# Kernel optimization log

Measured on AMD Instinct MI355X. Metric: run time of the kernel, lower is better.

Reference implementation:

```python
import jax, jax.numpy as jnp
import numpy as np

NUM_HEADS = 12

def _rotate_half(t):
    t1, t2 = jnp.split(t, 2, axis=-1)
    return jnp.concatenate([-t2, t1], axis=-1)

def _rope_apply(t, sin, cos):
    # t: [B,H,N,Dh]; sin/cos: [N,Dh] broadcast over B,H
    return t * cos + _rotate_half(t) * sin


def setup_inputs() -> dict:
    key = jax.random.key(0)
    ks = jax.random.split(key, 6)
    B, N, D = 2, 2048, 768
    Dh = D // NUM_HEADS
    return {
        "x": jax.random.normal(ks[0], (B, N, D), dtype=jnp.float32),
        "sin": jax.random.uniform(ks[1], (N, Dh), dtype=jnp.float32),
        "cos": jax.random.uniform(ks[2], (N, Dh), dtype=jnp.float32),
        "qkv_w": jax.random.normal(ks[3], (3 * D, D), dtype=jnp.float32) * (D ** -0.5),
        "proj_w": jax.random.normal(ks[4], (D, D), dtype=jnp.float32) * (D ** -0.5),
        "proj_b": jax.random.normal(ks[5], (D,), dtype=jnp.float32),
    }


def reference(x, sin, cos, qkv_w, proj_w, proj_b):
    B, N, D = x.shape
    H = NUM_HEADS
    Dh = D // H
    scale = Dh ** -0.5
    # fused QKV projection (qkv_bias=False)
    qkv = jnp.einsum("bnd,ed->bne", x, qkv_w)              # [B,N,3D]
    qkv = qkv.reshape(B, N, 3, H, Dh)
    q = jnp.transpose(qkv[:, :, 0], (0, 2, 1, 3))          # [B,H,N,Dh]
    k = jnp.transpose(qkv[:, :, 1], (0, 2, 1, 3))
    v = jnp.transpose(qkv[:, :, 2], (0, 2, 1, 3))
    # inline RoPE (prefix = 0: sin/cos cover all N positions)
    q = _rope_apply(q, sin, cos)
    k = _rope_apply(k, sin, cos)
    # scaled dot-product attention
    scores = jnp.einsum("bhqd,bhkd->bhqk", q, k) * scale   # [B,H,N,N]
    attn = jax.nn.softmax(scores, axis=-1)
    out = jnp.einsum("bhqk,bhkd->bhqd", attn, v)           # [B,H,N,Dh]
    out = jnp.transpose(out, (0, 2, 1, 3)).reshape(B, N, D)
    # output projection
    return jnp.einsum("bnd,ed->bne", out, proj_w) + proj_b
```

## Files before the change

kernel.cpp:

```cpp
#include <hip/hip_runtime.h>
#include <hip/hip_bf16.h>
#include <stdint.h>


typedef unsigned short u16;
typedef __attribute__((ext_vector_type(8))) short s16x8;
typedef __attribute__((ext_vector_type(4))) float f32x4;

#define MFMA16(a, b, c) __builtin_amdgcn_mfma_f32_16x16x32_bf16((a), (b), (c), 0, 0, 0)

__device__ __forceinline__ u16 f2bf(float f) {
    uint32_t u = __float_as_uint(f);
    u = u + 0x7fffu + ((u >> 16) & 1u);
    return (u16)(u >> 16);
}
__device__ __forceinline__ uint32_t pk2(float lo, float hi) {
    return (uint32_t)f2bf(lo) | ((uint32_t)f2bf(hi) << 16);
}
__device__ __forceinline__ float fexp2(float x) { return __builtin_amdgcn_exp2f(x); }

__device__ __forceinline__ void gload16(const void* g, void* l) {
    __builtin_amdgcn_global_load_lds(
        (const __attribute__((address_space(1))) unsigned int*)g,
        (__attribute__((address_space(3))) unsigned int*)l,
        16, 0, 0);
}

__global__ __launch_bounds__(256)
void k_cvt(const float* __restrict__ src, u16* __restrict__ dst, int n4)
{
    const int i = blockIdx.x * 256 + threadIdx.x;
    if (i < n4) {
        const float4 v = ((const float4*)src)[i];
        ushort4 o;
        o.x = f2bf(v.x); o.y = f2bf(v.y); o.z = f2bf(v.z); o.w = f2bf(v.w);
        ((ushort4*)dst)[i] = o;
    }
}

__global__ __launch_bounds__(256, 2)
void k_qkv_rope(const u16* __restrict__ X,
                const u16* __restrict__ W,
                const float* __restrict__ SIN,
                const float* __restrict__ COS,
                u16* __restrict__ qws, u16* __restrict__ kws, u16* __restrict__ vtws)
{
    __shared__ u16 smem[17408];
    u16* const As0 = smem;
    u16* const Bs0 = smem + 8192;

    const int t  = threadIdx.x;
    const int l  = t & 63;
    const int w  = t >> 6;
    const int cl = l & 15, gh = l >> 4;
    const int brow = blockIdx.x * 128;
    const int bcol = blockIdx.y * 128;
    const int wr = (w >> 1) * 64;
    const int wc = (w & 1) * 64;

    const int srow = w * 16 + (l >> 2);
    const int scol = (((l & 3) ^ ((l >> 3) & 3)) * 8);
    const u16* gA = X + (size_t)(brow + srow) * 768 + scol;
    const u16* gB = W + (size_t)(bcol + srow) * 768 + scol;

    const int csw = ((cl >> 1) & 3);

    f32x4 acc[4][4] = {};

    gload16(gA,            As0 + w * 512);
    gload16(gA + 64 * 768, As0 + 2048 + w * 512);
    gload16(gB,            Bs0 + w * 512);
    gload16(gB + 64 * 768, Bs0 + 2048 + w * 512);
    __syncthreads();

    for (int kt = 0; kt < 24; ++kt) {
        const int cur = kt & 1;
        if (kt + 1 < 24) {
            const int k0 = (kt + 1) * 32;
            u16* An = As0 + (cur ^ 1) * 4096;
            u16* Bn = Bs0 + (cur ^ 1) * 4096;
            gload16(gA + k0,            An + w * 512);
            gload16(gA + k0 + 64 * 768, An + 2048 + w * 512);
            gload16(gB + k0,            Bn + w * 512);
            gload16(gB + k0 + 64 * 768, Bn + 2048 + w * 512);
        }
        const char* Ac = (const char*)(As0 + cur * 4096);
        const char* Bc = (const char*)(Bs0 + cur * 4096);
        s16x8 af[4], bv[4];
        #pragma unroll
        for (int m = 0; m < 4; ++m) {
            const int row = wr + m * 16 + cl;
            af[m] = *(const s16x8*)(Ac + row * 64 + ((gh ^ csw) << 4));
        }
        #pragma unroll
        for (int n = 0; n < 4; ++n) {
            const int row = wc + n * 16 + cl;
            bv[n] = *(const s16x8*)(Bc + row * 64 + ((gh ^ csw) << 4));
        }
        #pragma unroll
        for (int m = 0; m < 4; ++m)
            #pragma unroll
            for (int n = 0; n < 4; ++n)
                acc[m][n] = MFMA16(af[m], bv[n], acc[m][n]);
        __syncthreads();
    }

    if (blockIdx.y >= 12) {
        u16* const Vt = smem;
        #pragma unroll
        for (int m = 0; m < 4; ++m)
            #pragma unroll
            for (int jj = 0; jj < 4; ++jj) {
                const int rowl = wr + m * 16 + gh * 4 + jj;
                #pragma unroll
                for (int n = 0; n < 4; ++n)
                    Vt[(wc + n * 16 + cl) * 136 + rowl] = f2bf(acc[m][n][jj]);
            }
        __syncthreads();
        const int dhcol = t >> 1;
        const int c     = t & 1;
        const int gcol  = bcol + dhcol;
        const int h     = (gcol >> 6) - 24;
        const int dh    = gcol & 63;
        const int b     = brow >> 11;
        const int tok0  = (brow & 2047) + c * 64;
        u16* dst = vtws + ((size_t)(b * 12 + h) * 64 + dh) * 2048 + tok0;
        const uint4* src = (const uint4*)((const char*)Vt + dhcol * 272 + c * 128);
        #pragma unroll
        for (int j = 0; j < 8; ++j)
            ((uint4*)dst)[j] = src[j];
    } else {
        const int seg   = (bcol + wc) >> 6;
        const int which = seg / 12;
        const int h     = seg % 12;
        const float qscl = (which == 0) ? 0.1803368801111244f : 1.0f;
        u16* outp = (which == 0) ? qws : kws;

        #pragma unroll
        for (int m = 0; m < 4; ++m) {
            #pragma unroll
            for (int jj = 0; jj < 4; ++jj) {
                const int row = brow + wr + m * 16 + gh * 4 + jj;
                const int b   = row >> 11;
                const int tok = row & 2047;
                u16* orow = outp + ((size_t)(b * 12 + h) * 2048 + tok) * 64;
                const float* srow2 = SIN + tok * 64;
                const float* crow2 = COS + tok * 64;
                #pragma unroll
                for (int n = 0; n < 4; ++n) {
                    const int dh = n * 16 + cl;
                    const float v = acc[m][n][jj];
                    const float partner = (n < 2) ? -acc[m][n + 2][jj] : acc[m][n - 2][jj];
                    orow[dh] = f2bf((v * crow2[dh] + partner * srow2[dh]) * qscl);
                }
            }
        }
    }
}

__global__ __launch_bounds__(256)
void k_attn(const u16* __restrict__ Qg, const u16* __restrict__ Kg,
            const u16* __restrict__ VTg, u16* __restrict__ Og)
{
    __shared__ u16 Ks[2][64 * 64];
    __shared__ u16 Vs[2][64 * 64];

    const int t  = threadIdx.x;
    const int l  = t & 63;
    const int w  = t >> 6;
    const int cl = l & 15, gh = l >> 4;

    const int i  = blockIdx.x;
    const int bh = (i & 7) * 3 + ((i >> 3) % 3);
    const int qt = i / 24;
    const int qb = qt * 64 + w * 16;

    const u16* Q  = Qg  + (size_t)bh * 2048 * 64;
    const char* Kb  = (const char*)(Kg  + (size_t)bh * 2048 * 64);
    const char* VTb = (const char*)(VTg + (size_t)bh * 64 * 2048);

    s16x8 qf[2];
    #pragma unroll
    for (int ks = 0; ks < 2; ++ks)
        qf[ks] = *(const s16x8*)(Q + (((qb + cl) << 6) + ks * 32 + gh * 8));

    f32x4 o[4] = {};
    float lrun = 0.f;

    const int srcA = cl + (gh & 1) * 32;
    const int srcB = srcA + 16;
    const bool loGH = (gh < 2);

    const int srow8 = l >> 3;
    const int scolb = (((l & 7) ^ srow8) << 4);

    const int rsw = (cl & 7) << 4;

    {
        #pragma unroll
        for (int c = 0; c < 2; ++c) {
            const int s = c * 4 + w;
            const int grow = s * 8 + srow8;
            gload16(Kb  + grow * 128 + scolb,  &Ks[0][s * 512]);
            gload16(VTb + grow * 4096 + scolb, &Vs[0][s * 512]);
        }
    }
    __syncthreads();

    for (int kt = 0; kt < 32; ++kt) {
        const int cur = kt & 1;

        if (kt + 1 < 32) {
            const int nb = (kt + 1) * 64;
            #pragma unroll
            for (int c = 0; c < 2; ++c) {
                const int s = c * 4 + w;
                const int grow = s * 8 + srow8;
                gload16(Kb  + (nb + grow) * 128 + scolb,    &Ks[cur ^ 1][s * 512]);
                gload16(VTb + grow * 4096 + nb * 2 + scolb, &Vs[cur ^ 1][s * 512]);
            }
        }

        const char* kl = (const char*)Ks[cur];
        const char* vl = (const char*)Vs[cur];
        s16x8 kf[4][2], vf[4][2];
        #pragma unroll
        for (int nk = 0; nk < 4; ++nk)
            #pragma unroll
            for (int ks = 0; ks < 2; ++ks)
                kf[nk][ks] = *(const s16x8*)(kl + (nk * 16 + cl) * 128 + ((ks * 64 + gh * 16) ^ rsw));
        #pragma unroll
        for (int n = 0; n < 4; ++n)
            #pragma unroll
            for (int ks = 0; ks < 2; ++ks)
                vf[n][ks] = *(const s16x8*)(vl + (n * 16 + cl) * 128 + ((ks * 64 + gh * 16) ^ rsw));

        f32x4 st[4] = {};
        #pragma unroll
        for (int nk = 0; nk < 4; ++nk)
            #pragma unroll
            for (int ks = 0; ks < 2; ++ks)
                st[nk] = MFMA16(kf[nk][ks], qf[ks], st[nk]);

        uint32_t d[4][2];
        float sum = 0.f;
        #pragma unroll
        for (int nk = 0; nk < 4; ++nk) {
            const float p0 = fexp2(st[nk][0] - 12.f);
            const float p1 = fexp2(st[nk][1] - 12.f);
            const float p2 = fexp2(st[nk][2] - 12.f);
            const float p3 = fexp2(st[nk][3] - 12.f);
            sum += (p0 + p1) + (p2 + p3);
            d[nk][0] = pk2(p0, p1);
            d[nk][1] = pk2(p2, p3);
        }
        lrun += sum;

        #pragma unroll
        for (int ks = 0; ks < 2; ++ks) {
            const uint32_t e0 = d[2 * ks][0],     e1 = d[2 * ks][1];
            const uint32_t q0 = d[2 * ks + 1][0], q1 = d[2 * ks + 1][1];
            const uint32_t xE0 = (uint32_t)__shfl((int)e0, srcA);
            const uint32_t xE1 = (uint32_t)__shfl((int)e1, srcA);
            const uint32_t xE2 = (uint32_t)__shfl((int)e0, srcB);
            const uint32_t xE3 = (uint32_t)__shfl((int)e1, srcB);
            const uint32_t xO0 = (uint32_t)__shfl((int)q0, srcA);
            const uint32_t xO1 = (uint32_t)__shfl((int)q1, srcA);
            const uint32_t xO2 = (uint32_t)__shfl((int)q0, srcB);
            const uint32_t xO3 = (uint32_t)__shfl((int)q1, srcB);
            union { s16x8 v; uint32_t u[4]; } pa;
            pa.u[0] = loGH ? xE0 : xO0;
            pa.u[1] = loGH ? xE1 : xO1;
            pa.u[2] = loGH ? xE2 : xO2;
            pa.u[3] = loGH ? xE3 : xO3;
            #pragma unroll
            for (int n = 0; n < 4; ++n)
                o[n] = MFMA16(vf[n][ks], pa.v, o[n]);
        }

        __syncthreads();
    }

    const int b = bh / 12, h = bh % 12;
    float lr = lrun;
    lr += __shfl_xor(lr, 16);
    lr += __shfl_xor(lr, 32);
    const float inv = 1.0f / lr;
    const int tok = qb + cl;
    u16* orow = Og + ((size_t)(b * 2048 + tok)) * 768 + h * 64;
    #pragma unroll
    for (int n = 0; n < 4; ++n) {
        uint2 pkv;
        pkv.x = pk2(o[n][0] * inv, o[n][1] * inv);
        pkv.y = pk2(o[n][2] * inv, o[n][3] * inv);
        *(uint2*)(orow + n * 16 + gh * 4) = pkv;
    }
}

__global__ __launch_bounds__(256, 2)
void k_proj(const u16* __restrict__ A,
            const u16* __restrict__ W,
            const float* __restrict__ BIAS,
            float* __restrict__ OUT)
{
    __shared__ u16 smem[16384];
    u16* const As0 = smem;
    u16* const Bs0 = smem + 8192;

    const int t  = threadIdx.x;
    const int l  = t & 63;
    const int w  = t >> 6;
    const int cl = l & 15, gh = l >> 4;
    const int brow = blockIdx.x * 128;
    const int bcol = blockIdx.y * 128;
    const int wr = (w >> 1) * 64;
    const int wc = (w & 1) * 64;

    const int srow = w * 16 + (l >> 2);
    const int scol = (((l & 3) ^ ((l >> 3) & 3)) * 8);
    const u16* gA = A + (size_t)(brow + srow) * 768 + scol;
    const u16* gB = W + (size_t)(bcol + srow) * 768 + scol;
    const int csw = ((cl >> 1) & 3);

    f32x4 acc[4][4] = {};

    gload16(gA,            As0 + w * 512);
    gload16(gA + 64 * 768, As0 + 2048 + w * 512);
    gload16(gB,            Bs0 + w * 512);
    gload16(gB + 64 * 768, Bs0 + 2048 + w * 512);
    __syncthreads();

    for (int kt = 0; kt < 24; ++kt) {
        const int cur = kt & 1;
        if (kt + 1 < 24) {
            const int k0 = (kt + 1) * 32;
            u16* An = As0 + (cur ^ 1) * 4096;
            u16* Bn = Bs0 + (cur ^ 1) * 4096;
            gload16(gA + k0,            An + w * 512);
            gload16(gA + k0 + 64 * 768, An + 2048 + w * 512);
            gload16(gB + k0,            Bn + w * 512);
            gload16(gB + k0 + 64 * 768, Bn + 2048 + w * 512);
        }
        const char* Ac = (const char*)(As0 + cur * 4096);
        const char* Bc = (const char*)(Bs0 + cur * 4096);
        s16x8 af[4], bv[4];
        #pragma unroll
        for (int m = 0; m < 4; ++m) {
            const int row = wr + m * 16 + cl;
            af[m] = *(const s16x8*)(Ac + row * 64 + ((gh ^ csw) << 4));
        }
        #pragma unroll
        for (int n = 0; n < 4; ++n) {
            const int row = wc + n * 16 + cl;
            bv[n] = *(const s16x8*)(Bc + row * 64 + ((gh ^ csw) << 4));
        }
        #pragma unroll
        for (int m = 0; m < 4; ++m)
            #pragma unroll
            for (int n = 0; n < 4; ++n)
                acc[m][n] = MFMA16(af[m], bv[n], acc[m][n]);
        __syncthreads();
    }

    #pragma unroll
    for (int m = 0; m < 4; ++m) {
        #pragma unroll
        for (int jj = 0; jj < 4; ++jj) {
            const int row = brow + wr + m * 16 + gh * 4 + jj;
            #pragma unroll
            for (int n = 0; n < 4; ++n) {
                const int col = bcol + wc + n * 16 + cl;
                OUT[(size_t)row * 768 + col] = acc[m][n][jj] + BIAS[col];
            }
        }
    }
}

extern "C" void kernel_launch(void* const* d_in, const int* in_sizes, int n_in,
                              void* d_out, int out_size, void* d_ws, size_t ws_size,
                              hipStream_t stream)
{
    const float* x     = (const float*)d_in[0];
    const float* sinp  = (const float*)d_in[1];
    const float* cosp  = (const float*)d_in[2];
    const float* qkv_w = (const float*)d_in[3];
    const float* projw = (const float*)d_in[4];
    const float* projb = (const float*)d_in[5];
    float* out = (float*)d_out;

    const size_t N_X  = (size_t)4096 * 768;
    const size_t N_WQ = (size_t)2304 * 768;
    const size_t N_WP = (size_t)768 * 768;
    const size_t SEG  = (size_t)2 * 12 * 2048 * 64;

    u16* xbf   = (u16*)d_ws;
    u16* wqkv  = xbf + N_X;
    u16* wproj = wqkv + N_WQ;
    u16* qws   = wproj + N_WP;
    u16* kws   = qws + SEG;
    u16* vtws  = kws + SEG;
    u16* aws   = vtws + SEG;

    k_cvt<<<(int)(N_X  / 4 + 255) / 256, 256, 0, stream>>>(x,     xbf,   (int)(N_X  / 4));
    k_cvt<<<(int)(N_WQ / 4 + 255) / 256, 256, 0, stream>>>(qkv_w, wqkv,  (int)(N_WQ / 4));
    k_cvt<<<(int)(N_WP / 4 + 255) / 256, 256, 0, stream>>>(projw, wproj, (int)(N_WP / 4));

    k_qkv_rope<<<dim3(32, 18), 256, 0, stream>>>(xbf, wqkv, sinp, cosp, qws, kws, vtws);
    k_attn    <<<768, 256, 0, stream>>>(qws, kws, vtws, aws);
    k_proj    <<<dim3(32, 6),  256, 0, stream>>>(aws, wproj, projb, out);
}
```

Baseline: 112.3 us.

## Merge bf16 conversion launches and load V fragments directly from global

Measured after the change: 147.1 us. 30.9% more time.

```diff
diff --git a/kernel.cpp b/kernel.cpp
--- a/kernel.cpp
+++ b/kernel.cpp
@@ -27,15 +27,20 @@
 }
 
 __global__ __launch_bounds__(256)
-void k_cvt(const float* __restrict__ src, u16* __restrict__ dst, int n4)
+void k_cvt3(const float* __restrict__ s0, const float* __restrict__ s1,
+            const float* __restrict__ s2, u16* __restrict__ dst,
+            int a, int ab, int tot)
 {
     const int i = blockIdx.x * 256 + threadIdx.x;
-    if (i < n4) {
-        const float4 v = ((const float4*)src)[i];
-        ushort4 o;
-        o.x = f2bf(v.x); o.y = f2bf(v.y); o.z = f2bf(v.z); o.w = f2bf(v.w);
-        ((ushort4*)dst)[i] = o;
-    }
+    if (i >= tot) return;
+    const float4* src;
+    if (i < a)       src = (const float4*)s0 + i;
+    else if (i < ab) src = (const float4*)s1 + (i - a);
+    else             src = (const float4*)s2 + (i - ab);
+    const float4 v = *src;
+    ushort4 o;
+    o.x = f2bf(v.x); o.y = f2bf(v.y); o.z = f2bf(v.z); o.w = f2bf(v.w);
+    ((ushort4*)dst)[i] = o;
 }
 
 __global__ __launch_bounds__(256, 2)
@@ -163,7 +168,6 @@
             const u16* __restrict__ VTg, u16* __restrict__ Og)
 {
     __shared__ u16 Ks[2][64 * 64];
-    __shared__ u16 Vs[2][64 * 64];
 
     const int t  = threadIdx.x;
     const int l  = t & 63;
@@ -175,9 +179,9 @@
     const int qt = i / 24;
     const int qb = qt * 64 + w * 16;
 
-    const u16* Q  = Qg  + (size_t)bh * 2048 * 64;
-    const char* Kb  = (const char*)(Kg  + (size_t)bh * 2048 * 64);
-    const char* VTb = (const char*)(VTg + (size_t)bh * 64 * 2048);
+    const u16* Q   = Qg  + (size_t)bh * 2048 * 64;
+    const char* Kb = (const char*)(Kg + (size_t)bh * 2048 * 64);
+    const u16* VTe = VTg + (size_t)bh * 64 * 2048 + cl * 2048 + gh * 8;
 
     s16x8 qf[2];
     #pragma unroll
@@ -193,17 +197,12 @@
 
     const int srow8 = l >> 3;
     const int scolb = (((l & 7) ^ srow8) << 4);
-
     const int rsw = (cl & 7) << 4;
 
-    {
-        #pragma unroll
-        for (int c = 0; c < 2; ++c) {
-            const int s = c * 4 + w;
-            const int grow = s * 8 + srow8;
-            gload16(Kb  + grow * 128 + scolb,  &Ks[0][s * 512]);
-            gload16(VTb + grow * 4096 + scolb, &Vs[0][s * 512]);
-        }
+    #pragma unroll
+    for (int c = 0; c < 2; ++c) {
+        const int s = c * 4 + w;
+        gload16(Kb + (s * 8 + srow8) * 128 + scolb, &Ks[0][s * 512]);
     }
     __syncthreads();
 
@@ -215,25 +214,24 @@
             #pragma unroll
             for (int c = 0; c < 2; ++c) {
                 const int s = c * 4 + w;
-                const int grow = s * 8 + srow8;
-                gload16(Kb  + (nb + grow) * 128 + scolb,    &Ks[cur ^ 1][s * 512]);
-                gload16(VTb + grow * 4096 + nb * 2 + scolb, &Vs[cur ^ 1][s * 512]);
+                gload16(Kb + (nb + s * 8 + srow8) * 128 + scolb, &Ks[cur ^ 1][s * 512]);
             }
         }
 
+        s16x8 vf[4][2];
+        #pragma unroll
+        for (int n = 0; n < 4; ++n)
+            #pragma unroll
+            for (int ks = 0; ks < 2; ++ks)
+                vf[n][ks] = *(const s16x8*)(VTe + n * 32768 + kt * 64 + ks * 32);
+
         const char* kl = (const char*)Ks[cur];
-        const char* vl = (const char*)Vs[cur];
-        s16x8 kf[4][2], vf[4][2];
+        s16x8 kf[4][2];
         #pragma unroll
         for (int nk = 0; nk < 4; ++nk)
             #pragma unroll
             for (int ks = 0; ks < 2; ++ks)
                 kf[nk][ks] = *(const s16x8*)(kl + (nk * 16 + cl) * 128 + ((ks * 64 + gh * 16) ^ rsw));
-        #pragma unroll
-        for (int n = 0; n < 4; ++n)
-            #pragma unroll
-            for (int ks = 0; ks < 2; ++ks)
-                vf[n][ks] = *(const s16x8*)(vl + (n * 16 + cl) * 128 + ((ks * 64 + gh * 16) ^ rsw));
 
         f32x4 st[4] = {};
         #pragma unroll
@@ -401,9 +399,10 @@
     u16* vtws  = kws + SEG;
     u16* aws   = vtws + SEG;
 
-    k_cvt<<<(int)(N_X  / 4 + 255) / 256, 256, 0, stream>>>(x,     xbf,   (int)(N_X  / 4));
-    k_cvt<<<(int)(N_WQ / 4 + 255) / 256, 256, 0, stream>>>(qkv_w, wqkv,  (int)(N_WQ / 4));
-    k_cvt<<<(int)(N_WP / 4 + 255) / 256, 256, 0, stream>>>(projw, wproj, (int)(N_WP / 4));
+    const int a   = (int)(N_X / 4);
+    const int ab  = (int)((N_X + N_WQ) / 4);
+    const int tot = (int)((N_X + N_WQ + N_WP) / 4);
+    k_cvt3<<<(tot + 255) / 256, 256, 0, stream>>>(x, qkv_w, projw, xbf, a, ab, tot);
 
     k_qkv_rope<<<dim3(32, 18), 256, 0, stream>>>(xbf, wqkv, sinp, cosp, qws, kws, vtws);
     k_attn    <<<768, 256, 0, stream>>>(qws, kws, vtws, aws);
```
